# Optimization experiments

Measured on AMD Instinct MI355X. Metric: run time of the kernel, lower is better.

The kernel has to match this reference:

```python
import jax, jax.numpy as jnp
import numpy as np

HIDDEN_DIM = 256
ATTN_DIM = 256


def setup_inputs() -> dict:
    key = jax.random.key(0)
    k1, k2, k3, k4, k5, k6 = jax.random.split(key, 6)
    B, S, C, H, W = 16, 32, HIDDEN_DIM, 16, 16
    hidden_state = jax.random.normal(k1, (B, C, H, W), dtype=jnp.float32)
    encoder_outputs = jax.random.normal(k2, (B, S, C, H, W), dtype=jnp.float32)
    # 1x1 conv weights stored as [out_ch, in_ch] (kernel spatial dims are 1)
    W1 = jax.random.normal(k3, (ATTN_DIM, 2 * C), dtype=jnp.float32) * (1.0 / np.sqrt(2 * C))
    b1 = jax.random.normal(k4, (ATTN_DIM,), dtype=jnp.float32) * 0.01
    W2 = jax.random.normal(k5, (1, ATTN_DIM), dtype=jnp.float32) * (1.0 / np.sqrt(ATTN_DIM))
    b2 = jax.random.normal(k6, (1,), dtype=jnp.float32) * 0.01
    return {"hidden_state": hidden_state, "encoder_outputs": encoder_outputs,
            "W1": W1, "b1": b1, "W2": W2, "b2": b2}


def reference(hidden_state, encoder_outputs, W1, b1, W2, b2):
    # hidden_state: [B, C, H, W]; encoder_outputs: [B, S, C, H, W]
    C = hidden_state.shape[1]
    # conv1(cat(h_expanded, e)) decomposed: W1 = [W1h | W1e] over channel dim.
    W1h, W1e = W1[:, :C], W1[:, C:]
    # [B, A, H, W] broadcast over S + [B, S, A, H, W]
    eh = jnp.einsum('ac,bchw->bahw', W1h, hidden_state)
    ee = jnp.einsum('ac,bschw->bsahw', W1e, encoder_outputs)
    t = jnp.tanh(eh[:, None] + ee + b1[None, None, :, None, None])
    # conv2 -> [B, S, H, W], then spatial mean -> [B, S]
    energy = jnp.einsum('a,bsahw->bshw', W2[0], t) + b2[0]
    energy = energy.reshape(energy.shape[0], energy.shape[1], -1).mean(axis=2)
    attn_weights = jax.nn.softmax(energy, axis=1)  # [B, S]
    context = jnp.einsum('bs,bschw->bchw', attn_weights, encoder_outputs)
    return context
```

## Files before the change

### kernel.cpp

```cpp
#include <hip/hip_runtime.h>

#define P 256
#define CDIM 256
#define SDIM 32

typedef __attribute__((ext_vector_type(8))) short short8;
typedef __attribute__((ext_vector_type(4))) float f32x4;
typedef __attribute__((ext_vector_type(4))) unsigned int uint4v;

__device__ inline unsigned int pack2bf(float lo, float hi) {
    unsigned int ul = __builtin_bit_cast(unsigned int, lo);
    unsigned int uh = __builtin_bit_cast(unsigned int, hi);
    ul += 0x7fffu + ((ul >> 16) & 1u);
    uh += 0x7fffu + ((uh >> 16) & 1u);
    return (ul >> 16) | (uh & 0xffff0000u);
}

__global__ __launch_bounds__(256) void prep_kernel(const float* __restrict__ hid,
                                                   const float* __restrict__ W1,
                                                   const float* __restrict__ b1,
                                                   float* __restrict__ ehb1,
                                                   uint4v* __restrict__ packA) {
    const int blk = blockIdx.x;
    const int tid = threadIdx.x;
    if (blk >= 512) {
        const int t  = (blk - 512) * 256 + tid;
        const int a  = ((t >> 9) << 4) | (t & 15);
        const int kc = (t >> 4) & 31;
        const float* src = W1 + (size_t)a * 512 + 256 + kc * 8;
        const float4 f0 = *(const float4*)src;
        const float4 f1 = *(const float4*)(src + 4);
        uint4v u;
        u.x = pack2bf(f0.x, f0.y);
        u.y = pack2bf(f0.z, f0.w);
        u.z = pack2bf(f1.x, f1.y);
        u.w = pack2bf(f1.z, f1.w);
        packA[t] = u;
        return;
    }
    const int b  = blk >> 5;
    const int a0 = (blk & 31) << 3;
    const int p  = tid;
    float acc[8];
#pragma unroll
    for (int i = 0; i < 8; ++i) acc[i] = 0.f;
    const float* hb = hid + (size_t)b * CDIM * P;
    for (int c = 0; c < CDIM; c += 8) {
        float hv[8];
#pragma unroll
        for (int j = 0; j < 8; ++j) hv[j] = hb[(c + j) * P + p];
#pragma unroll
        for (int i = 0; i < 8; ++i) {
            const float* wr = W1 + (size_t)(a0 + i) * 512 + c;
#pragma unroll
            for (int j = 0; j < 8; ++j) acc[i] = fmaf(wr[j], hv[j], acc[i]);
        }
    }
#pragma unroll
    for (int i = 0; i < 8; ++i)
        ehb1[((size_t)b * CDIM + a0 + i) * P + p] = acc[i] + b1[a0 + i];
}

__global__ __launch_bounds__(256, 3) void energy_mfma(const float* __restrict__ enc,
                                                      const unsigned char* __restrict__ packA,
                                                      const float* __restrict__ W2,
                                                      const float* __restrict__ ehb1,
                                                      float* __restrict__ partial) {
    __shared__ __align__(16) unsigned char ldsF[64 * 256];
    __shared__ __align__(16) unsigned char ldsB[2][64 * 128];
    __shared__ float red[4];
    const int bid = blockIdx.x;
    const int bs  = bid >> 2;
    const int pq  = bid & 3;
    const int b   = bs >> 5;
    const int tid = threadIdx.x;
    const int l   = tid & 63;
    const int w   = tid >> 6;
    const int g   = l >> 4;
    const int i16 = l & 15;
    const int a_base = w * 64;
    const int cg4 = tid >> 4;
    const int p4  = tid & 15;
    const int p_r = tid & 63;
    const int ch  = tid >> 6;
    const float* eb = enc + (size_t)bs * (CDIM * P) + pq * 64;
    const float* ehbB = ehb1 + (size_t)b * (CDIM * P) + pq * 64;

    float4 gv0[4];
#pragma unroll
    for (int r = 0; r < 4; ++r)
        gv0[r] = *(const float4*)(eb + (size_t)(r * 16 + cg4) * P + p4 * 4);
    __builtin_amdgcn_sched_barrier(0);

    f32x4 acc[4][4];
    float w2v[4][4];
#pragma unroll
    for (int m = 0; m < 4; ++m) {
#pragma unroll
        for (int r = 0; r < 4; ++r) {
            const int a = a_base + m * 16 + g * 4 + r;
            w2v[m][r] = W2[a];
            const float* ehr = ehbB + (size_t)a * P + i16;
#pragma unroll
            for (int n = 0; n < 4; ++n)
                acc[m][n][r] = ehr[n * 16];
        }
    }
    __builtin_amdgcn_sched_barrier(0);

#pragma unroll
    for (int r = 0; r < 4; ++r) {
        const int c = r * 16 + cg4;
        *(float4*)(ldsF + c * 256 + ((p4 * 16) ^ ((c & 7) << 4))) = gv0[r];
    }
    __syncthreads();
    {
        float cv[16];
#pragma unroll
        for (int j = 0; j < 16; ++j) {
            const int c = ch * 16 + j;
            cv[j] = *(const float*)(ldsF + c * 256 +
                     ((((p_r >> 2) * 16) ^ ((c & 7) << 4)) | ((p_r & 3) * 4)));
        }
        unsigned char* dst = ldsB[0] + p_r * 128;
#pragma unroll
        for (int h = 0; h < 2; ++h) {
            uint4v u;
            u.x = pack2bf(cv[h*8+0], cv[h*8+1]);
            u.y = pack2bf(cv[h*8+2], cv[h*8+3]);
            u.z = pack2bf(cv[h*8+4], cv[h*8+5]);
            u.w = pack2bf(cv[h*8+6], cv[h*8+7]);
            *(uint4v*)(dst + ((ch * 32 + h * 16) ^ ((p_r & 7) << 4))) = u;
        }
    }
    __syncthreads();

#pragma unroll
    for (int kt = 0; kt < 4; ++kt) {
        short8 af[2][4];
#pragma unroll
        for (int kh = 0; kh < 2; ++kh)
#pragma unroll
            for (int m = 0; m < 4; ++m) {
                const int chunk = ((a_base >> 4) + m) * 32 + kt * 8 + kh * 4;
                af[kh][m] = __builtin_bit_cast(short8,
                    *(const uint4v*)(packA + (size_t)chunk * 256 + l * 16));
            }
        __builtin_amdgcn_sched_barrier(0);
        float4 gv[4];
        if (kt < 3) {
#pragma unroll
            for (int r = 0; r < 4; ++r)
                gv[r] = *(const float4*)(eb + (size_t)((kt + 1) * 64 + r * 16 + cg4) * P + p4 * 4);
        }
#pragma unroll
        for (int kh = 0; kh < 2; ++kh) {
            short8 bf[4];
#pragma unroll
            for (int n = 0; n < 4; ++n) {
                const int row = n * 16 + i16;
                bf[n] = __builtin_bit_cast(short8,
                    *(const uint4v*)(ldsB[kt & 1] + row * 128 +
                                     (((kh * 4 + g) * 16) ^ ((row & 7) << 4))));
            }
#pragma unroll
            for (int m = 0; m < 4; ++m)
#pragma unroll
                for (int n = 0; n < 4; ++n)
                    acc[m][n] = __builtin_amdgcn_mfma_f32_16x16x32_bf16(af[kh][m], bf[n], acc[m][n], 0, 0, 0);
        }
        if (kt < 3) {
#pragma unroll
            for (int r = 0; r < 4; ++r) {
                const int c = r * 16 + cg4;
                *(float4*)(ldsF + c * 256 + ((p4 * 16) ^ ((c & 7) << 4))) = gv[r];
            }
            __syncthreads();
            float cv[16];
#pragma unroll
            for (int j = 0; j < 16; ++j) {
                const int c = ch * 16 + j;
                cv[j] = *(const float*)(ldsF + c * 256 +
                         ((((p_r >> 2) * 16) ^ ((c & 7) << 4)) | ((p_r & 3) * 4)));
            }
            unsigned char* dst = ldsB[(kt + 1) & 1] + p_r * 128;
#pragma unroll
            for (int h = 0; h < 2; ++h) {
                uint4v u;
                u.x = pack2bf(cv[h*8+0], cv[h*8+1]);
                u.y = pack2bf(cv[h*8+2], cv[h*8+3]);
                u.z = pack2bf(cv[h*8+4], cv[h*8+5]);
                u.w = pack2bf(cv[h*8+6], cv[h*8+7]);
                *(uint4v*)(dst + ((ch * 32 + h * 16) ^ ((p_r & 7) << 4))) = u;
            }
            __syncthreads();
        }
    }

    float epm[4];
#pragma unroll
    for (int m = 0; m < 4; ++m) {
        float e = 0.f;
#pragma unroll
        for (int r = 0; r < 4; ++r) {
            const float wv = w2v[m][r];
#pragma unroll
            for (int n = 0; n < 4; ++n) {
                const float x  = acc[m][n][r];
                const float ex = __expf(2.f * x);
                const float t  = 1.f - 2.f / (ex + 1.f);
                e = fmaf(wv, t, e);
            }
        }
        epm[m] = e;
    }
    float ep = (epm[0] + epm[1]) + (epm[2] + epm[3]);
#pragma unroll
    for (int off = 32; off > 0; off >>= 1) ep += __shfl_down(ep, off, 64);
    if (l == 0) red[w] = ep;
    __syncthreads();
    if (tid == 0)
        partial[(size_t)bs * 4 + pq] = red[0] + red[1] + red[2] + red[3];
}

__global__ __launch_bounds__(256) void context_kernel(const float4* __restrict__ enc4,
                                                      const float* __restrict__ partial,
                                                      const float* __restrict__ b2,
                                                      float4* __restrict__ out4) {
    const int bi = blockIdx.x;
    const int b  = bi >> 6;
    const int i4 = ((bi & 63) << 8) + threadIdx.x;

    float e[SDIM];
    const float* pb = partial + (size_t)b * SDIM * 4;
    const float bias = b2[0];
#pragma unroll
    for (int s = 0; s < SDIM; ++s)
        e[s] = (pb[s*4] + pb[s*4+1] + pb[s*4+2] + pb[s*4+3]) * (1.f / 256.f) + bias;
    float m = e[0];
#pragma unroll
    for (int s = 1; s < SDIM; ++s) m = fmaxf(m, e[s]);
    float sum = 0.f;
#pragma unroll
    for (int s = 0; s < SDIM; ++s) { e[s] = __expf(e[s] - m); sum += e[s]; }
    const float inv = 1.f / sum;

    float4 acc = {0.f, 0.f, 0.f, 0.f};
    const float4* eb = enc4 + (size_t)b * SDIM * 16384 + i4;
#pragma unroll 4
    for (int s = 0; s < SDIM; ++s) {
        const float wv = e[s] * inv;
        const float4 v = eb[(size_t)s * 16384];
        acc.x = fmaf(wv, v.x, acc.x);
        acc.y = fmaf(wv, v.y, acc.y);
        acc.z = fmaf(wv, v.z, acc.z);
        acc.w = fmaf(wv, v.w, acc.w);
    }
    out4[(size_t)b * 16384 + i4] = acc;
}

extern "C" void kernel_launch(void* const* d_in, const int* in_sizes, int n_in,
                              void* d_out, int out_size, void* d_ws, size_t ws_size,
                              hipStream_t stream) {
    const float* hid = (const float*)d_in[0];
    const float* enc = (const float*)d_in[1];
    const float* W1  = (const float*)d_in[2];
    const float* b1  = (const float*)d_in[3];
    const float* W2  = (const float*)d_in[4];
    const float* b2  = (const float*)d_in[5];
    float* out = (float*)d_out;

    float* ehb1    = out;
    float* partial = (float*)d_ws;
    unsigned char* packA = (unsigned char*)(partial + 2048);

    prep_kernel<<<544, 256, 0, stream>>>(hid, W1, b1, ehb1, (uint4v*)packA);
    energy_mfma<<<2048, 256, 0, stream>>>(enc, packA, W2, ehb1, partial);
    context_kernel<<<1024, 256, 0, stream>>>((const float4*)enc, partial, b2, (float4*)out);
}
```

Measured before the change: 88.28 us.

## Issue all encoder loads upfront and convert whole tile before MFMA loop

The energy kernel now issues all 16 float4 global loads of its encoder tile at the start, then converts the whole 256-channel slice to bf16 in LDS before running the MFMA loop. This replaces the double-buffered load/convert pipeline that ran alongside the MFMAs. The aim is to expose more memory-level parallelism and take the conversion and barriers out of the compute loop. In exchange it raises register and LDS use, lowers the occupancy hint from 3 to 2, and drops the overlap of loads with compute. Separately, the prep kernel's blocks now each compute 4 attention channels instead of 8, doubling its grid.

```diff
diff --git a/kernel.cpp b/kernel.cpp
--- a/kernel.cpp
+++ b/kernel.cpp
@@ -23,8 +23,8 @@
                                                    uint4v* __restrict__ packA) {
     const int blk = blockIdx.x;
     const int tid = threadIdx.x;
-    if (blk >= 512) {
-        const int t  = (blk - 512) * 256 + tid;
+    if (blk >= 1024) {
+        const int t  = (blk - 1024) * 256 + tid;
         const int a  = ((t >> 9) << 4) | (t & 15);
         const int kc = (t >> 4) & 31;
         const float* src = W1 + (size_t)a * 512 + 256 + kc * 8;
@@ -38,36 +38,36 @@
         packA[t] = u;
         return;
     }
-    const int b  = blk >> 5;
-    const int a0 = (blk & 31) << 3;
+    const int b  = blk >> 6;
+    const int a0 = (blk & 63) << 2;
     const int p  = tid;
-    float acc[8];
-#pragma unroll
-    for (int i = 0; i < 8; ++i) acc[i] = 0.f;
+    float acc[4];
+#pragma unroll
+    for (int i = 0; i < 4; ++i) acc[i] = 0.f;
     const float* hb = hid + (size_t)b * CDIM * P;
     for (int c = 0; c < CDIM; c += 8) {
         float hv[8];
 #pragma unroll
         for (int j = 0; j < 8; ++j) hv[j] = hb[(c + j) * P + p];
 #pragma unroll
-        for (int i = 0; i < 8; ++i) {
+        for (int i = 0; i < 4; ++i) {
             const float* wr = W1 + (size_t)(a0 + i) * 512 + c;
 #pragma unroll
             for (int j = 0; j < 8; ++j) acc[i] = fmaf(wr[j], hv[j], acc[i]);
         }
     }
 #pragma unroll
-    for (int i = 0; i < 8; ++i)
+    for (int i = 0; i < 4; ++i)
         ehb1[((size_t)b * CDIM + a0 + i) * P + p] = acc[i] + b1[a0 + i];
 }
 
-__global__ __launch_bounds__(256, 3) void energy_mfma(const float* __restrict__ enc,
+__global__ __launch_bounds__(256, 2) void energy_mfma(const float* __restrict__ enc,
                                                       const unsigned char* __restrict__ packA,
                                                       const float* __restrict__ W2,
                                                       const float* __restrict__ ehb1,
                                                       float* __restrict__ partial) {
     __shared__ __align__(16) unsigned char ldsF[64 * 256];
-    __shared__ __align__(16) unsigned char ldsB[2][64 * 128];
+    __shared__ __align__(16) unsigned char ldsB[64 * 512];
     __shared__ float red[4];
     const int bid = blockIdx.x;
     const int bs  = bid >> 2;
@@ -83,13 +83,15 @@
     const int p4  = tid & 15;
     const int p_r = tid & 63;
     const int ch  = tid >> 6;
-    const float* eb = enc + (size_t)bs * (CDIM * P) + pq * 64;
-    const float* ehbB = ehb1 + (size_t)b * (CDIM * P) + pq * 64;
-
-    float4 gv0[4];
-#pragma unroll
-    for (int r = 0; r < 4; ++r)
-        gv0[r] = *(const float4*)(eb + (size_t)(r * 16 + cg4) * P + p4 * 4);
+    const float* eb   = enc  + (size_t)bs * (CDIM * P) + pq * 64;
+    const float* ehbB = ehb1 + (size_t)b  * (CDIM * P) + pq * 64;
+
+    float4 gv[4][4];
+#pragma unroll
+    for (int kt = 0; kt < 4; ++kt)
+#pragma unroll
+        for (int r = 0; r < 4; ++r)
+            gv[kt][r] = *(const float4*)(eb + (size_t)(kt * 64 + r * 16 + cg4) * P + p4 * 4);
     __builtin_amdgcn_sched_barrier(0);
 
     f32x4 acc[4][4];
@@ -109,12 +111,13 @@
     __builtin_amdgcn_sched_barrier(0);
 
 #pragma unroll
-    for (int r = 0; r < 4; ++r) {
-        const int c = r * 16 + cg4;
-        *(float4*)(ldsF + c * 256 + ((p4 * 16) ^ ((c & 7) << 4))) = gv0[r];
-    }
-    __syncthreads();
-    {
+    for (int kt = 0; kt < 4; ++kt) {
+#pragma unroll
+        for (int r = 0; r < 4; ++r) {
+            const int c = r * 16 + cg4;
+            *(float4*)(ldsF + c * 256 + ((p4 * 16) ^ ((c & 7) << 4))) = gv[kt][r];
+        }
+        __syncthreads();
         float cv[16];
 #pragma unroll
         for (int j = 0; j < 16; ++j) {
@@ -122,7 +125,7 @@
             cv[j] = *(const float*)(ldsF + c * 256 +
                      ((((p_r >> 2) * 16) ^ ((c & 7) << 4)) | ((p_r & 3) * 4)));
         }
-        unsigned char* dst = ldsB[0] + p_r * 128;
+        unsigned char* dst = ldsB + p_r * 512;
 #pragma unroll
         for (int h = 0; h < 2; ++h) {
             uint4v u;
@@ -130,10 +133,10 @@
             u.y = pack2bf(cv[h*8+2], cv[h*8+3]);
             u.z = pack2bf(cv[h*8+4], cv[h*8+5]);
             u.w = pack2bf(cv[h*8+6], cv[h*8+7]);
-            *(uint4v*)(dst + ((ch * 32 + h * 16) ^ ((p_r & 7) << 4))) = u;
-        }
-    }
-    __syncthreads();
+            *(uint4v*)(dst + ((kt * 128 + ch * 32 + h * 16) ^ ((p_r & 7) << 4))) = u;
+        }
+        __syncthreads();
+    }
 
 #pragma unroll
     for (int kt = 0; kt < 4; ++kt) {
@@ -146,13 +149,6 @@
                 af[kh][m] = __builtin_bit_cast(short8,
                     *(const uint4v*)(packA + (size_t)chunk * 256 + l * 16));
             }
-        __builtin_amdgcn_sched_barrier(0);
-        float4 gv[4];
-        if (kt < 3) {
-#pragma unroll
-            for (int r = 0; r < 4; ++r)
-                gv[r] = *(const float4*)(eb + (size_t)((kt + 1) * 64 + r * 16 + cg4) * P + p4 * 4);
-        }
 #pragma unroll
         for (int kh = 0; kh < 2; ++kh) {
             short8 bf[4];
@@ -160,40 +156,14 @@
             for (int n = 0; n < 4; ++n) {
                 const int row = n * 16 + i16;
                 bf[n] = __builtin_bit_cast(short8,
-                    *(const uint4v*)(ldsB[kt & 1] + row * 128 +
-                                     (((kh * 4 + g) * 16) ^ ((row & 7) << 4))));
+                    *(const uint4v*)(ldsB + row * 512 +
+                        ((kt * 128 + (kh * 4 + g) * 16) ^ ((row & 7) << 4))));
             }
 #pragma unroll
             for (int m = 0; m < 4; ++m)
 #pragma unroll
                 for (int n = 0; n < 4; ++n)
                     acc[m][n] = __builtin_amdgcn_mfma_f32_16x16x32_bf16(af[kh][m], bf[n], acc[m][n], 0, 0, 0);
-        }
-        if (kt < 3) {
-#pragma unroll
-            for (int r = 0; r < 4; ++r) {
-                const int c = r * 16 + cg4;
-                *(float4*)(ldsF + c * 256 + ((p4 * 16) ^ ((c & 7) << 4))) = gv[r];
-            }
-            __syncthreads();
-            float cv[16];
-#pragma unroll
-            for (int j = 0; j < 16; ++j) {
-                const int c = ch * 16 + j;
-                cv[j] = *(const float*)(ldsF + c * 256 +
-                         ((((p_r >> 2) * 16) ^ ((c & 7) << 4)) | ((p_r & 3) * 4)));
-            }
-            unsigned char* dst = ldsB[(kt + 1) & 1] + p_r * 128;
-#pragma unroll
-            for (int h = 0; h < 2; ++h) {
-                uint4v u;
-                u.x = pack2bf(cv[h*8+0], cv[h*8+1]);
-                u.y = pack2bf(cv[h*8+2], cv[h*8+3]);
-                u.z = pack2bf(cv[h*8+4], cv[h*8+5]);
-                u.w = pack2bf(cv[h*8+6], cv[h*8+7]);
-                *(uint4v*)(dst + ((ch * 32 + h * 16) ^ ((p_r & 7) << 4))) = u;
-            }
-            __syncthreads();
         }
     }
 
@@ -274,7 +244,7 @@
     float* partial = (float*)d_ws;
     unsigned char* packA = (unsigned char*)(partial + 2048);
 
-    prep_kernel<<<544, 256, 0, stream>>>(hid, W1, b1, ehb1, (uint4v*)packA);
+    prep_kernel<<<1056, 256, 0, stream>>>(hid, W1, b1, ehb1, (uint4v*)packA);
     energy_mfma<<<2048, 256, 0, stream>>>(enc, packA, W2, ehb1, partial);
     context_kernel<<<1024, 256, 0, stream>>>((const float4*)enc, partial, b2, (float4*)out);
 }
```

Result: slower. 121.7 us (+37.8%).
